# Kernel tuning notes

Hardware: AMD Instinct MI355X
Metric: run time of the kernel (lower is better)

Reference implementation:

```python
import jax, jax.numpy as jnp
import numpy as np

B, L, NV = 16, 512, 64
D = 512
PATCH_LEN, STRIDE, PADDING = 16, 8, 8
N_PATCH = (L - PATCH_LEN) // STRIDE + 2  # 64
PRED = 192
MEM = 8192
TOPK = 8
NHEAD = 4
NORM_CONST = 0.4
HEAD_NF = D * N_PATCH


def _pos_emb(n, d):
    pos = np.arange(n)[:, None].astype(np.float32)
    div = np.exp(np.arange(0, d, 2).astype(np.float32) * (-np.log(10000.0) / d))
    pe = np.zeros((n, d), np.float32)
    pe[:, 0::2] = np.sin(pos * div)
    pe[:, 1::2] = np.cos(pos * div)
    return jnp.asarray(pe)

POS = _pos_emb(N_PATCH, D)


def gelu(x):
    return jax.nn.gelu(x, approximate=False)  # torch nn.GELU default = exact erf


def setup_inputs() -> dict:
    key = jax.random.key(0)
    ks = jax.random.split(key, 16)
    s = lambda i, shape, scale=0.02: jax.random.normal(ks[i], shape, jnp.float32) * scale
    return dict(
        x_enc=jax.random.normal(ks[0], (B, L, NV), jnp.float32),
        W_val=s(1, (PATCH_LEN, D), 0.05),
        mem_bank=s(2, (MEM, D), 1.0),
        W_m1=s(3, (D, 2 * D)), b_m1=jnp.zeros((2 * D,), jnp.float32),
        W_m2=s(4, (2 * D, D)), b_m2=jnp.zeros((D,), jnp.float32),
        W_q=s(5, (D, D)), b_q=jnp.zeros((D,), jnp.float32),
        W_k=s(6, (D, D)), b_k=jnp.zeros((D,), jnp.float32),
        W_v=s(7, (D, D)), b_v=jnp.zeros((D,), jnp.float32),
        W_o=s(8, (D, D)), b_o=jnp.zeros((D,), jnp.float32),
        W_g1=s(9, (2 * D, D)), b_g1=jnp.zeros((D,), jnp.float32),
        W_g2=s(10, (D, 2)), b_g2=jnp.zeros((2,), jnp.float32),
        W_h=s(11, (HEAD_NF, PRED)), b_h=jnp.zeros((PRED,), jnp.float32),
        W_f1=s(12, (PRED, 2 * PRED)), b_f1=jnp.zeros((2 * PRED,), jnp.float32),
        W_f2=s(13, (2 * PRED, PRED)), b_f2=jnp.zeros((PRED,), jnp.float32),
    )


def reference(x_enc, W_val, mem_bank, W_m1, b_m1, W_m2, b_m2,
              W_q, b_q, W_k, b_k, W_v, b_v, W_o, b_o,
              W_g1, b_g1, W_g2, b_g2, W_h, b_h, W_f1, b_f1, W_f2, b_f2):
    # instance normalization over the time axis (means detached in torch)
    means = jax.lax.stop_gradient(jnp.mean(x_enc, axis=1, keepdims=True))
    xc = x_enc - means
    stdev = jnp.sqrt(jnp.var(xc, axis=1, keepdims=True) + 1e-5) / NORM_CONST
    x = xc / stdev                                              # [B, L, NV]

    # patch embedding: replication pad at end, unfold, linear + sinusoidal pos
    xt = jnp.transpose(x, (0, 2, 1))                            # [B, NV, L]
    xt = jnp.concatenate([xt, jnp.repeat(xt[..., -1:], PADDING, axis=-1)], axis=-1)
    win = (jnp.arange(N_PATCH) * STRIDE)[:, None] + jnp.arange(PATCH_LEN)  # [N, P]
    patches = xt[..., win].reshape(B * NV, N_PATCH, PATCH_LEN)  # [BN, N, P]
    emb = patches @ W_val + POS                                 # [BN, N, D]

    # local memory: mean-pooled query -> matmul similarity -> top-k gather -> MLP
    qflat = jnp.mean(emb, axis=1)                               # [BN, D]
    sim = qflat @ mem_bank.T                                    # [BN, MEM]
    _, idx = jax.lax.top_k(sim, TOPK)                           # [BN, K]
    retr = mem_bank[idx]                                        # [BN, K, D]
    h = gelu(retr @ W_m1 + b_m1) @ W_m2 + b_m2
    local = jnp.mean(h, axis=1, keepdims=True) + emb            # [BN, N, D]

    # global memory: multihead self-attention (4 heads, batch_first)
    dh = D // NHEAD
    heads = lambda t: t.reshape(B * NV, N_PATCH, NHEAD, dh).transpose(0, 2, 1, 3)
    q = heads(emb @ W_q + b_q)
    k = heads(emb @ W_k + b_k)
    v = heads(emb @ W_v + b_v)
    att = jax.nn.softmax(jnp.einsum('bhqd,bhkd->bhqk', q, k) / jnp.sqrt(jnp.float32(dh)), axis=-1)
    glob = jnp.einsum('bhqk,bhkd->bhqd', att, v).transpose(0, 2, 1, 3).reshape(B * NV, N_PATCH, D)
    glob = glob @ W_o + b_o                                     # [BN, N, D]

    # gated fusion of local/global memory
    comb = jnp.concatenate([local, glob], axis=-1)              # [BN, N, 2D]
    gate = jax.nn.softmax(gelu(comb @ W_g1 + b_g1) @ W_g2 + b_g2, axis=-1)
    mem = gate[..., 0:1] * local + gate[..., 1:2] * glob        # [BN, N, D]

    # flatten -> memory head -> fusion layer with residual
    flat = mem.reshape(B * NV, HEAD_NF)
    mh = (flat @ W_h + b_h).reshape(B, NV, PRED)
    pred = gelu(gelu(mh @ W_f1 + b_f1) @ W_f2 + b_f2) + mh
    pred = jnp.transpose(pred, (0, 2, 1))                       # [B, PRED, NV]

    # denormalize
    return pred * stdev + means
```

## Files before the change

kernel.cpp:

```cpp
#include <hip/hip_runtime.h>
#include <stdint.h>

#define DEV __device__ __forceinline__

typedef uint16_t u16;
typedef __bf16 bf16x8 __attribute__((ext_vector_type(8)));
typedef float f32x4 __attribute__((ext_vector_type(4)));
typedef u16 u16x8 __attribute__((ext_vector_type(8)));

DEV float bf2f(u16 v) { return __uint_as_float(((uint32_t)v) << 16); }
DEV u16 f2bf(float f) {
  uint32_t u = __float_as_uint(f);
  u += 0x7fffu + ((u >> 16) & 1u);
  return (u16)(u >> 16);
}
DEV float gelu_f(float x) { return 0.5f * x * (1.0f + erff(x * 0.7071067811865475f)); }

DEV void gload_lds16(const u16* g, u16* l) {
  __builtin_amdgcn_global_load_lds(
      (const __attribute__((address_space(1))) void*)g,
      (__attribute__((address_space(3))) void*)l, 16, 0, 0);
}

struct __align__(16) Scratch {
  float POSb[64 * 512];
  float meanv[1024];
  float stdv[1024];
  float mh[1024 * 192];
  int idxB[8192];
  float qflat[1024 * 512];
  float gatel[65536 * 2];
  float bqkv[1536];
  u16 hmeanB[1024 * 512];
  u16 gmeanB[1024 * 1024];
  u16 WqkvT[1536 * 512];
  u16 WoT[512 * 512];
  u16 Wm1T[1024 * 512];
  u16 Wm2T[512 * 1024];
  u16 Wg1T[512 * 1024];
  u16 WhT[256 * 32768];
  u16 memdupB[8192 * 1536];
  u16 embh[65536 * 512];
  u16 qkvb[65536 * 1536];
};
__device__ Scratch g_s;

__global__ __launch_bounds__(256) void zerof_kernel(float* __restrict__ p, int n) {
  int t = blockIdx.x * 256 + threadIdx.x;
  if (t < n) p[t] = 0.f;
}
__global__ __launch_bounds__(256) void zerou8_kernel(u16* __restrict__ p, int n8) {
  int t = blockIdx.x * 256 + threadIdx.x;
  if (t < n8) *(u16x8*)(p + (long)t * 8) = (u16x8)0;
}
__global__ __launch_bounds__(256) void biasqkv_kernel(const float* __restrict__ bq,
                                                      const float* __restrict__ bk,
                                                      const float* __restrict__ bv,
                                                      float* __restrict__ o) {
  int t = blockIdx.x * 256 + threadIdx.x;
  o[t] = t < 512 ? bq[t] : (t < 1024 ? bk[t - 512] : bv[t - 1024]);
}

__global__ __launch_bounds__(256) void pos_kernel(float* __restrict__ POS) {
  int n = blockIdx.x;
  int i = threadIdx.x;
  float div = expf((float)(2 * i) * (-9.210340371976184f / 512.0f));
  float arg = (float)n * div;
  POS[n * 512 + 2 * i] = sinf(arg);
  POS[n * 512 + 2 * i + 1] = cosf(arg);
}

__global__ __launch_bounds__(256) void stats_kernel(const float* __restrict__ x_enc,
                                                    float* __restrict__ meanv,
                                                    float* __restrict__ stdv) {
  int b = blockIdx.x;
  int v = threadIdx.x & 63;
  int g = threadIdx.x >> 6;
  float s = 0.f, s2 = 0.f;
  for (int l = g; l < 512; l += 4) {
    float x = x_enc[((long)b * 512 + l) * 64 + v];
    s += x; s2 += x * x;
  }
  __shared__ float sh[2][4][64];
  sh[0][g][v] = s; sh[1][g][v] = s2;
  __syncthreads();
  if (g == 0) {
    s = sh[0][0][v] + sh[0][1][v] + sh[0][2][v] + sh[0][3][v];
    s2 = sh[1][0][v] + sh[1][1][v] + sh[1][2][v] + sh[1][3][v];
    float mu = s * (1.f / 512.f);
    float var = s2 * (1.f / 512.f) - mu * mu;
    meanv[b * 64 + v] = mu;
    stdv[b * 64 + v] = sqrtf(var + 1e-5f) * 2.5f;
  }
}

__global__ __launch_bounds__(256) void transpose_kernel(const float* __restrict__ in,
                                                        u16* __restrict__ out, int R, int C) {
  __shared__ u16 t[32][33];
  int bx = blockIdx.x * 32;
  int by = blockIdx.y * 32;
  int tx = threadIdx.x & 31, ty = threadIdx.x >> 5;
  for (int i = ty; i < 32; i += 8) t[i][tx] = f2bf(in[(long)(by + i) * C + bx + tx]);
  __syncthreads();
  for (int i = ty; i < 32; i += 8) out[(long)(bx + i) * R + by + tx] = t[tx][i];
}

__global__ __launch_bounds__(256) void emb_kernel(const float* __restrict__ x_enc,
                                                  const float* __restrict__ W_val,
                                                  const float* __restrict__ POS,
                                                  const float* __restrict__ meanv,
                                                  const float* __restrict__ stdv,
                                                  u16* __restrict__ embh,
                                                  u16* __restrict__ qsC) {
  int bn = blockIdx.x;
  int b = bn >> 6, v = bn & 63;
  int tid = threadIdx.x;
  __shared__ __align__(16) float wv[16 * 512];
  __shared__ __align__(16) float pt[64 * 16];
  for (int i = tid; i < 8192; i += 256) wv[i] = W_val[i];
  float mu = meanv[bn];
  float inv = 1.f / stdv[bn];
  for (int i = tid; i < 1024; i += 256) {
    int n = i >> 4, p = i & 15;
    int l = n * 8 + p; if (l > 511) l = 511;
    pt[i] = (x_enc[((long)b * 512 + l) * 64 + v] - mu) * inv;
  }
  __syncthreads();
  float qs0 = 0.f, qs1 = 0.f;
  int d0 = tid, d1 = tid + 256;
  for (int n = 0; n < 64; ++n) {
    float a0 = POS[n * 512 + d0], a1 = POS[n * 512 + d1];
#pragma unroll
    for (int p = 0; p < 16; ++p) {
      float pv = pt[n * 16 + p];
      a0 += pv * wv[p * 512 + d0];
      a1 += pv * wv[p * 512 + d1];
    }
    long base = ((long)bn * 64 + n) * 512;
    embh[base + d0] = f2bf(a0);
    embh[base + d1] = f2bf(a1);
    qs0 += a0; qs1 += a1;
  }
  float q0 = qs0 * (1.f / 64.f), q1 = qs1 * (1.f / 64.f);
  u16 h0 = f2bf(q0), l0 = f2bf(q0 - bf2f(h0));
  u16 h1 = f2bf(q1), l1 = f2bf(q1 - bf2f(h1));
  long qb = (long)bn * 1536;
  qsC[qb + d0] = h0; qsC[qb + 512 + d0] = l0; qsC[qb + 1024 + d0] = h0;
  qsC[qb + d1] = h1; qsC[qb + 512 + d1] = l1; qsC[qb + 1024 + d1] = h1;
}

__global__ __launch_bounds__(256) void memdup_kernel(const float* __restrict__ mb,
                                                     u16* __restrict__ md) {
  int t = blockIdx.x * 256 + threadIdx.x;
  int n = t >> 6, k8 = (t & 63) * 8;
  const float* src = mb + (long)n * 512 + k8;
  u16x8 hi, lo;
#pragma unroll
  for (int z = 0; z < 8; ++z) {
    float m = src[z];
    u16 h = f2bf(m);
    hi[z] = h;
    lo[z] = f2bf(m - bf2f(h));
  }
  long base = (long)n * 1536 + k8;
  *(u16x8*)(md + base) = hi;
  *(u16x8*)(md + base + 512) = hi;
  *(u16x8*)(md + base + 1024) = lo;
}

template <int EPI>
__global__ __launch_bounds__(256) void gemm_nt(const u16* __restrict__ Ag,
                                               const u16* __restrict__ Bt,
                                               const float* __restrict__ bias,
                                               void* __restrict__ C,
                                               int lda, int ldb, int K, int Nreal, int ldc,
                                               int nT, long zstride) {
  __shared__ __align__(16) u16 smem[2 * 128 * 64];
  u16* As = smem;
  u16* Bs = smem + 8192;
  const int tid = threadIdx.x;
  const int id = blockIdx.x;
  const int xcd = id & 7;
  const int kk = id >> 3;
  const long bm = (long)((kk / nT) * 8 + xcd) * 128;
  const long bnn = (long)(kk % nT) * 128;
  const long koff = (long)blockIdx.z * K;
  const int lane = tid & 63;
  const int w = tid >> 6;
  const int wm = (w & 1) * 64;
  const int wn = (w >> 1) * 64;
  const int r16 = lane & 15;
  const int q4 = lane >> 4;

  f32x4 acc[4][4] = {};

  const u16* ap[4];
  const u16* bp[4];
  u16* al[4];
  u16* bl[4];
#pragma unroll
  for (int j = 0; j < 4; ++j) {
    int cid = (j * 4 + w) * 64 + lane;
    int r = cid >> 3;
    int g = (cid & 7) ^ (r & 7);
    ap[j] = Ag + (bm + r) * lda + koff + g * 8;
    bp[j] = Bt + (bnn + r) * ldb + koff + g * 8;
    al[j] = As + cid * 8;
    bl[j] = Bs + cid * 8;
  }

  for (int k0 = 0; k0 < K; k0 += 64) {
#pragma unroll
    for (int j = 0; j < 4; ++j) gload_lds16(ap[j] + k0, al[j]);
#pragma unroll
    for (int j = 0; j < 4; ++j) gload_lds16(bp[j] + k0, bl[j]);
    __syncthreads();
#pragma unroll
    for (int sub = 0; sub < 2; ++sub) {
      const int gg = q4 + sub * 4;
      bf16x8 av[4], bv[4];
#pragma unroll
      for (int i = 0; i < 4; ++i) {
        int r = wm + i * 16 + r16;
        av[i] = *reinterpret_cast<const bf16x8*>(As + (r * 8 + (gg ^ (r & 7))) * 8);
      }
#pragma unroll
      for (int j2 = 0; j2 < 4; ++j2) {
        int r = wn + j2 * 16 + r16;
        bv[j2] = *reinterpret_cast<const bf16x8*>(Bs + (r * 8 + (gg ^ (r & 7))) * 8);
      }
#pragma unroll
      for (int i = 0; i < 4; ++i)
#pragma unroll
        for (int j2 = 0; j2 < 4; ++j2)
          acc[i][j2] = __builtin_amdgcn_mfma_f32_16x16x32_bf16(av[i], bv[j2], acc[i][j2], 0, 0, 0);
    }
    __syncthreads();
  }

  if (EPI == 3) {
    float* Cz = (float*)C + (long)blockIdx.z * zstride;
    float* epf = (float*)smem + w * 2048;
#pragma unroll
    for (int half = 0; half < 2; ++half) {
#pragma unroll
      for (int i = 0; i < 2; ++i)
#pragma unroll
        for (int j = 0; j < 4; ++j)
#pragma unroll
          for (int r = 0; r < 4; ++r)
            epf[(i * 16 + q4 * 4 + r) * 64 + j * 16 + r16] = acc[half * 2 + i][j][r];
      __syncthreads();
#pragma unroll
      for (int v2 = 0; v2 < 8; ++v2) {
        int idx = v2 * 64 + lane;
        int row = idx >> 4, c4 = (idx & 15) * 4;
        f32x4 vec = *(const f32x4*)(epf + row * 64 + c4);
        long grow = bm + wm + half * 32 + row;
        int gcol = (int)bnn + wn + c4;
        if (gcol < Nreal) *(f32x4*)(Cz + grow * (long)ldc + gcol) = vec;
      }
      __syncthreads();
    }
  } else {
    u16* ep = smem + w * 2304;
    float bcol[4];
#pragma unroll
    for (int j = 0; j < 4; ++j) bcol[j] = bias[bnn + wn + j * 16 + r16];
#pragma unroll
    for (int half = 0; half < 2; ++half) {
#pragma unroll
      for (int i = 0; i < 2; ++i)
#pragma unroll
        for (int j = 0; j < 4; ++j)
#pragma unroll
          for (int r = 0; r < 4; ++r) {
            float v = acc[half * 2 + i][j][r] + bcol[j];
            if (EPI == 1) v = gelu_f(v);
            ep[(i * 16 + q4 * 4 + r) * 72 + j * 16 + r16] = f2bf(v);
          }
      __syncthreads();
#pragma unroll
      for (int v2 = 0; v2 < 4; ++v2) {
        int row = v2 * 8 + (lane >> 3);
        int c8 = (lane & 7) * 8;
        u16x8 vec = *(const u16x8*)(ep + row * 72 + c8);
        long grow = bm + wm + half * 32 + row;
        int gcol = (int)bnn + wn + c8;
        if (gcol < Nreal) *(u16x8*)((u16*)C + grow * (long)ldc + gcol) = vec;
      }
      __syncthreads();
    }
  }
}

DEV bool better(float v1, int i1, float v2, int i2) {
  return v1 > v2 || (v1 == v2 && i1 < i2);
}
__global__ __launch_bounds__(256) void topk_kernel(const float* __restrict__ sim,
                                                   int* __restrict__ idxout) {
  const int bn = blockIdx.x;
  const int tid = threadIdx.x;
  const float* row = sim + (long)bn * 8192;
  float bv[8]; int bi[8];
#pragma unroll
  for (int r = 0; r < 8; ++r) { bv[r] = -3.0e38f; bi[r] = 0x7fffffff; }
  for (int n = tid; n < 8192; n += 256) {
    float v = row[n];
    if (better(v, n, bv[7], bi[7])) {
      bv[7] = v; bi[7] = n;
      for (int r = 7; r > 0; --r) {
        if (!better(bv[r], bi[r], bv[r - 1], bi[r - 1])) break;
        float tv = bv[r]; bv[r] = bv[r - 1]; bv[r - 1] = tv;
        int ti = bi[r]; bi[r] = bi[r - 1]; bi[r - 1] = ti;
      }
    }
  }
  __shared__ float lv[256 * 8];
  __shared__ int li[256 * 8];
#pragma unroll
  for (int r = 0; r < 8; ++r) { lv[tid * 8 + r] = bv[r]; li[tid * 8 + r] = bi[r]; }
  __syncthreads();
  for (int step = 128; step >= 1; step >>= 1) {
    if (tid < step) {
      float av[8], xv[8]; int ai[8], xi[8];
#pragma unroll
      for (int r = 0; r < 8; ++r) {
        av[r] = lv[tid * 8 + r]; ai[r] = li[tid * 8 + r];
        xv[r] = lv[(tid + step) * 8 + r]; xi[r] = li[(tid + step) * 8 + r];
      }
      int ia = 0, ib = 0;
      float mv[8]; int mi[8];
#pragma unroll
      for (int r = 0; r < 8; ++r) {
        if (better(av[ia], ai[ia], xv[ib], xi[ib])) { mv[r] = av[ia]; mi[r] = ai[ia]; ++ia; }
        else { mv[r] = xv[ib]; mi[r] = xi[ib]; ++ib; }
      }
#pragma unroll
      for (int r = 0; r < 8; ++r) { lv[tid * 8 + r] = mv[r]; li[tid * 8 + r] = mi[r]; }
    }
    __syncthreads();
  }
  if (tid < 8) idxout[bn * 8 + tid] = li[tid];
}

__global__ __launch_bounds__(256) void gather_kernel(const float* __restrict__ mb,
                                                     const int* __restrict__ idx,
                                                     u16* __restrict__ retrB) {
  int t = blockIdx.x * 256 + threadIdx.x;
  int m = t >> 6;
  int c8 = (t & 63) * 8;
  long r = idx[m];
  if (r < 0) r = 0;
  if (r > 8191) r = 8191;
  const float* src = mb + r * 512 + c8;
  u16x8 o;
#pragma unroll
  for (int z = 0; z < 8; ++z) o[z] = f2bf(src[z]);
  *(u16x8*)(retrB + (long)m * 512 + c8) = o;
}

__global__ __launch_bounds__(256) void gmean_kernel(const u16* __restrict__ hid,
                                                    u16* __restrict__ gmeanB) {
  int t = blockIdx.x * 256 + threadIdx.x;
  int bn = t >> 7, j8 = (t & 127) * 8;
  float s[8] = {};
#pragma unroll
  for (int k = 0; k < 8; ++k) {
    u16x8 v = *(const u16x8*)(hid + (long)(bn * 8 + k) * 1024 + j8);
#pragma unroll
    for (int z = 0; z < 8; ++z) s[z] += bf2f(v[z]);
  }
  u16x8 o;
#pragma unroll
  for (int z = 0; z < 8; ++z) o[z] = f2bf(s[z] * 0.125f);
  *(u16x8*)(gmeanB + (long)bn * 1024 + j8) = o;
}

__global__ __launch_bounds__(256) void attn_kernel(u16* __restrict__ qkvb) {
  __shared__ __align__(16) u16 smem[26752];
  u16* Qs = smem;
  u16* Ks = smem + 8704;
  float* ss = (float*)(smem + 8704);
  u16* ps = smem;
  u16* Os = smem;
  u16* Vb = smem + 17408;
  float* red = (float*)(smem + 25728);
  const int bn = blockIdx.x, h = blockIdx.y;
  const int tid = threadIdx.x;
  const int lane = tid & 63, w = tid >> 6;
  const int r16 = lane & 15, q4 = lane >> 4;
  const long base = (long)bn * 64 * 1536 + h * 128;

  for (int c = tid; c < 1024; c += 256) {
    int r = c >> 4, c8 = (c & 15) * 8;
    u16x8 vq = *(const u16x8*)(qkvb + base + (long)r * 1536 + c8);
    u16x8 vk = *(const u16x8*)(qkvb + base + (long)r * 1536 + 512 + c8);
    u16x8 vv = *(const u16x8*)(qkvb + base + (long)r * 1536 + 1024 + c8);
    *(u16x8*)(Qs + r * 136 + c8) = vq;
    *(u16x8*)(Ks + r * 136 + c8) = vk;
    int kt = r >> 5, q4t = (r >> 3) & 3, e = r & 7;
    int nt = c8 >> 4, rb = c8 & 15;
    int vbase = (nt * 2 + kt) * 520 + (q4t * 16 + rb) * 8 + e;
#pragma unroll
    for (int z = 0; z < 8; ++z) Vb[vbase + z * 8] = vv[z];
  }
  __syncthreads();

  const int m0 = w * 16;
  f32x4 accS[4] = {};
#pragma unroll
  for (int k0 = 0; k0 < 128; k0 += 32) {
    bf16x8 av = *(const bf16x8*)(Qs + (m0 + r16) * 136 + k0 + q4 * 8);
#pragma unroll
    for (int j = 0; j < 4; ++j) {
      bf16x8 bvf = *(const bf16x8*)(Ks + (j * 16 + r16) * 136 + k0 + q4 * 8);
      accS[j] = __builtin_amdgcn_mfma_f32_16x16x32_bf16(av, bvf, accS[j], 0, 0, 0);
    }
  }
  __syncthreads();
  const float scale = 0.08838834764831845f;
#pragma unroll
  for (int j = 0; j < 4; ++j)
#pragma unroll
    for (int r = 0; r < 4; ++r)
      ss[(m0 + q4 * 4 + r) * 66 + j * 16 + r16] = accS[j][r] * scale;
  __syncthreads();

  {
    int r = tid >> 2, p = tid & 3;
    float* row = ss + r * 66 + p * 16;
    float mx = -3.0e38f;
#pragma unroll
    for (int c2 = 0; c2 < 16; ++c2) mx = fmaxf(mx, row[c2]);
    red[r * 4 + p] = mx;
    __syncthreads();
    float m4 = fmaxf(fmaxf(red[r * 4], red[r * 4 + 1]),
                     fmaxf(red[r * 4 + 2], red[r * 4 + 3]));
    float s = 0.f;
#pragma unroll
    for (int c2 = 0; c2 < 16; ++c2) {
      float e = expf(row[c2] - m4);
      row[c2] = e;
      s += e;
    }
    red[256 + r * 4 + p] = s;
    __syncthreads();
    float inv = 1.f / (red[256 + r * 4] + red[256 + r * 4 + 1] +
                       red[256 + r * 4 + 2] + red[256 + r * 4 + 3]);
    u16x8 o0, o1;
#pragma unroll
    for (int z = 0; z < 8; ++z) {
      o0[z] = f2bf(row[z] * inv);
      o1[z] = f2bf(row[8 + z] * inv);
    }
    *(u16x8*)(ps + r * 72 + p * 16) = o0;
    *(u16x8*)(ps + r * 72 + p * 16 + 8) = o1;
  }
  __syncthreads();

  bf16x8 av0 = *(const bf16x8*)(ps + (m0 + r16) * 72 + q4 * 8);
  bf16x8 av1 = *(const bf16x8*)(ps + (m0 + r16) * 72 + 32 + q4 * 8);
  __syncthreads();
#pragma unroll
  for (int nt = 0; nt < 8; ++nt) {
    f32x4 accO = {};
    bf16x8 bv0 = *(const bf16x8*)(Vb + (nt * 2 + 0) * 520 + lane * 8);
    bf16x8 bv1 = *(const bf16x8*)(Vb + (nt * 2 + 1) * 520 + lane * 8);
    accO = __builtin_amdgcn_mfma_f32_16x16x32_bf16(av0, bv0, accO, 0, 0, 0);
    accO = __builtin_amdgcn_mfma_f32_16x16x32_bf16(av1, bv1, accO, 0, 0, 0);
#pragma unroll
    for (int r = 0; r < 4; ++r) {
      int i = m0 + q4 * 4 + r;
      int col = nt * 16 + r16;
      Os[i * 128 + (col ^ (q4 << 4))] = f2bf(accO[r]);
    }
  }
  __syncthreads();
#pragma unroll
  for (int z = 0; z < 4; ++z) {
    int idx = z * 256 + tid;
    int row = idx >> 4, c8 = (idx & 15) * 8;
    int c8s = c8 ^ (((row >> 2) & 3) << 4);
    u16x8 vec = *(const u16x8*)(Os + row * 128 + c8s);
    *(u16x8*)(qkvb + base + (long)row * 1536 + c8) = vec;
  }
}

__global__ __launch_bounds__(256) void local_kernel(u16* __restrict__ embh,
                                                    const u16* __restrict__ hmeanB) {
  long t = (long)blockIdx.x * 256 + threadIdx.x;
  long e8 = t * 8;
  long m = e8 >> 9;
  int d = (int)(e8 & 511);
  int bn = (int)(m >> 6);
  u16x8 a = *(const u16x8*)(embh + e8);
  u16x8 b = *(const u16x8*)(hmeanB + (long)bn * 512 + d);
  u16x8 o;
#pragma unroll
  for (int z = 0; z < 8; ++z) o[z] = f2bf(bf2f(a[z]) + bf2f(b[z]));
  *(u16x8*)(embh + e8) = o;
}

__global__ __launch_bounds__(256) void gemm_cat(const u16* __restrict__ A1,
                                                const u16* __restrict__ A2,
                                                const u16* __restrict__ Bt,
                                                const float* __restrict__ bias,
                                                const float* __restrict__ W_g2,
                                                float* __restrict__ gatel,
                                                int lda1, int lda2, int nT) {
  __shared__ __align__(16) u16 smem[2 * 128 * 64];
  u16* As = smem;
  u16* Bs = smem + 8192;
  const int tid = threadIdx.x;
  const int id = blockIdx.x;
  const int xcd = id & 7;
  const int kk = id >> 3;
  const long bm = (long)((kk / nT) * 8 + xcd) * 128;
  const long bnn = (long)(kk % nT) * 128;
  const int lane = tid & 63;
  const int w = tid >> 6;
  const int wm = (w & 1) * 64;
  const int wn = (w >> 1) * 64;
  const int r16 = lane & 15;
  const int q4 = lane >> 4;

  f32x4 acc[4][4] = {};

  const u16* ap1[4];
  const u16* ap2[4];
  const u16* bp[4];
  u16* al[4];
  u16* bl[4];
#pragma unroll
  for (int j = 0; j < 4; ++j) {
    int cid = (j * 4 + w) * 64 + lane;
    int r = cid >> 3;
    int g = (cid & 7) ^ (r & 7);
    ap1[j] = A1 + (bm + r) * lda1 + g * 8;
    ap2[j] = A2 + (bm + r) * lda2 + g * 8;
    bp[j] = Bt + (bnn + r) * 1024 + g * 8;
    al[j] = As + cid * 8;
    bl[j] = Bs + cid * 8;
  }

  for (int k0 = 0; k0 < 1024; k0 += 64) {
    if (k0 < 512) {
#pragma unroll
      for (int j = 0; j < 4; ++j) gload_lds16(ap1[j] + k0, al[j]);
    } else {
#pragma unroll
      for (int j = 0; j < 4; ++j) gload_lds16(ap2[j] + (k0 - 512), al[j]);
    }
#pragma unroll
    for (int j = 0; j < 4; ++j) gload_lds16(bp[j] + k0, bl[j]);
    __syncthreads();
#pragma unroll
    for (int sub = 0; sub < 2; ++sub) {
      const int gg = q4 + sub * 4;
      bf16x8 av[4], bv[4];
#pragma unroll
      for (int i = 0; i < 4; ++i) {
        int r = wm + i * 16 + r16;
        av[i] = *reinterpret_cast<const bf16x8*>(As + (r * 8 + (gg ^ (r & 7))) * 8);
      }
#pragma unroll
      for (int j2 = 0; j2 < 4; ++j2) {
        int r = wn + j2 * 16 + r16;
        bv[j2] = *reinterpret_cast<const bf16x8*>(Bs + (r * 8 + (gg ^ (r & 7))) * 8);
      }
#pragma unroll
      for (int i = 0; i < 4; ++i)
#pragma unroll
        for (int j2 = 0; j2 < 4; ++j2)
          acc[i][j2] = __builtin_amdgcn_mfma_f32_16x16x32_bf16(av[i], bv[j2], acc[i][j2], 0, 0, 0);
    }
    __syncthreads();
  }

  float bcol[4], w0[4], w1[4];
#pragma unroll
  for (int j = 0; j < 4; ++j) {
    int gc = (int)bnn + wn + j * 16 + r16;
    bcol[j] = bias[gc];
    w0[j] = W_g2[gc * 2];
    w1[j] = W_g2[gc * 2 + 1];
  }
#pragma unroll
  for (int i = 0; i < 4; ++i)
#pragma unroll
    for (int r = 0; r < 4; ++r) {
      float a0 = 0.f, a1 = 0.f;
#pragma unroll
      for (int j = 0; j < 4; ++j) {
        float h = gelu_f(acc[i][j][r] + bcol[j]);
        a0 += h * w0[j];
        a1 += h * w1[j];
      }
#pragma unroll
      for (int off = 1; off < 16; off <<= 1) {
        a0 += __shfl_xor(a0, off);
        a1 += __shfl_xor(a1, off);
      }
      if (r16 == 0) {
        long row = bm + wm + i * 16 + q4 * 4 + r;
        atomicAdd(&gatel[row * 2], a0);
        atomicAdd(&gatel[row * 2 + 1], a1);
      }
    }
}

__global__ __launch_bounds__(256) void memc_kernel(u16* __restrict__ embh,
                                                   const u16* __restrict__ qkvb,
                                                   const float* __restrict__ gatel,
                                                   const float* __restrict__ b_g2) {
  long t = (long)blockIdx.x * 256 + threadIdx.x;
  long e8 = t * 8;
  long m = e8 >> 9;
  int d = (int)(e8 & 511);
  float l0 = gatel[m * 2] + b_g2[0];
  float l1 = gatel[m * 2 + 1] + b_g2[1];
  float mx = fmaxf(l0, l1);
  float e0 = expf(l0 - mx), e1 = expf(l1 - mx);
  float inv = 1.f / (e0 + e1);
  float g0 = e0 * inv, g1 = e1 * inv;
  u16x8 loc = *(const u16x8*)(embh + e8);
  u16x8 gl = *(const u16x8*)(qkvb + m * 1536 + 512 + d);
  u16x8 o;
#pragma unroll
  for (int z = 0; z < 8; ++z) o[z] = f2bf(g0 * bf2f(loc[z]) + g1 * bf2f(gl[z]));
  *(u16x8*)(embh + e8) = o;
}

__global__ __launch_bounds__(256) void fusion_kernel(const float* __restrict__ mh16,
                                                     const float* __restrict__ b_h,
                                                     const float* __restrict__ W_f1,
                                                     const float* __restrict__ b_f1,
                                                     const float* __restrict__ W_f2,
                                                     const float* __restrict__ b_f2,
                                                     const float* __restrict__ meanv,
                                                     const float* __restrict__ stdv,
                                                     float* __restrict__ out) {
  int bn = blockIdx.x;
  int tid = threadIdx.x;
  __shared__ float mrow[192];
  __shared__ float h1[384];
  if (tid < 192) {
    float a = b_h[tid];
#pragma unroll
    for (int z = 0; z < 16; ++z) a += mh16[(long)z * 196608 + (long)bn * 192 + tid];
    mrow[tid] = a;
  }
  __syncthreads();
  for (int j = tid; j < 384; j += 256) {
    float a = b_f1[j];
    for (int i = 0; i < 192; ++i) a += mrow[i] * W_f1[i * 384 + j];
    h1[j] = gelu_f(a);
  }
  __syncthreads();
  if (tid < 192) {
    float a = b_f2[tid];
    for (int j = 0; j < 384; ++j) a += h1[j] * W_f2[j * 192 + tid];
    float o = gelu_f(a) + mrow[tid];
    int b = bn >> 6, v = bn & 63;
    out[((long)b * 192 + tid) * 64 + v] = o * stdv[bn] + meanv[bn];
  }
}

extern "C" void kernel_launch(void* const* d_in, const int* in_sizes, int n_in,
                              void* d_out, int out_size, void* d_ws, size_t ws_size,
                              hipStream_t stream) {
  (void)in_sizes; (void)n_in; (void)out_size; (void)d_ws; (void)ws_size;
  const float* x_enc = (const float*)d_in[0];
  const float* W_val = (const float*)d_in[1];
  const float* mem_bank = (const float*)d_in[2];
  const float* W_m1 = (const float*)d_in[3];
  const float* b_m1 = (const float*)d_in[4];
  const float* W_m2 = (const float*)d_in[5];
  const float* b_m2 = (const float*)d_in[6];
  const float* W_q = (const float*)d_in[7];
  const float* b_q = (const float*)d_in[8];
  const float* W_k = (const float*)d_in[9];
  const float* b_k = (const float*)d_in[10];
  const float* W_v = (const float*)d_in[11];
  const float* b_v = (const float*)d_in[12];
  const float* W_o = (const float*)d_in[13];
  const float* b_o = (const float*)d_in[14];
  const float* W_g1 = (const float*)d_in[15];
  const float* b_g1 = (const float*)d_in[16];
  const float* W_g2 = (const float*)d_in[17];
  const float* b_g2 = (const float*)d_in[18];
  const float* W_h = (const float*)d_in[19];
  const float* b_h = (const float*)d_in[20];
  const float* W_f1 = (const float*)d_in[21];
  const float* b_f1 = (const float*)d_in[22];
  const float* W_f2 = (const float*)d_in[23];
  const float* b_f2 = (const float*)d_in[24];

  void* sp = nullptr;
  hipGetSymbolAddress(&sp, HIP_SYMBOL(g_s));
  Scratch* S = (Scratch*)sp;
  float* simB = (float*)S->qkvb;
  u16* qsC = S->qkvb + (size_t)16 * 1024 * 1024;
  u16* retrB = S->qkvb + (size_t)18 * 1024 * 1024;
  u16* hiddenB = S->qkvb + (size_t)24 * 1024 * 1024;
  float* mh16 = (float*)S->qkvb;

  pos_kernel<<<64, 256, 0, stream>>>(S->POSb);
  stats_kernel<<<16, 256, 0, stream>>>(x_enc, S->meanv, S->stdv);
  zerof_kernel<<<512, 256, 0, stream>>>(S->gatel, 65536 * 2);
  zerou8_kernel<<<1024, 256, 0, stream>>>(S->WhT + (size_t)192 * 32768, 64 * 32768 / 8);
  biasqkv_kernel<<<6, 256, 0, stream>>>(b_q, b_k, b_v, S->bqkv);
  transpose_kernel<<<dim3(16, 16), 256, 0, stream>>>(W_q, S->WqkvT, 512, 512);
  transpose_kernel<<<dim3(16, 16), 256, 0, stream>>>(W_k, S->WqkvT + 512 * 512, 512, 512);
  transpose_kernel<<<dim3(16, 16), 256, 0, stream>>>(W_v, S->WqkvT + 2 * 512 * 512, 512, 512);
  transpose_kernel<<<dim3(16, 16), 256, 0, stream>>>(W_o, S->WoT, 512, 512);
  transpose_kernel<<<dim3(32, 16), 256, 0, stream>>>(W_m1, S->Wm1T, 512, 1024);
  transpose_kernel<<<dim3(16, 32), 256, 0, stream>>>(W_m2, S->Wm2T, 1024, 512);
  transpose_kernel<<<dim3(16, 32), 256, 0, stream>>>(W_g1, S->Wg1T, 1024, 512);
  transpose_kernel<<<dim3(6, 1024), 256, 0, stream>>>(W_h, S->WhT, 32768, 192);
  memdup_kernel<<<2048, 256, 0, stream>>>(mem_bank, S->memdupB);

  emb_kernel<<<1024, 256, 0, stream>>>(x_enc, W_val, S->POSb, S->meanv, S->stdv,
                                       S->embh, qsC);
  gemm_nt<3><<<512, 256, 0, stream>>>(qsC, S->memdupB, nullptr, simB,
                                      1536, 1536, 1536, 8192, 8192, 64, 0L);
  topk_kernel<<<1024, 256, 0, stream>>>(simB, S->idxB);
  gather_kernel<<<2048, 256, 0, stream>>>(mem_bank, S->idxB, retrB);
  gemm_nt<1><<<512, 256, 0, stream>>>(retrB, S->Wm1T, b_m1, hiddenB,
                                      512, 512, 512, 1024, 1024, 8, 0L);
  gmean_kernel<<<512, 256, 0, stream>>>(hiddenB, S->gmeanB);
  gemm_nt<0><<<32, 256, 0, stream>>>(S->gmeanB, S->Wm2T, b_m2, S->hmeanB,
                                     1024, 1024, 1024, 512, 512, 4, 0L);
  gemm_nt<0><<<6144, 256, 0, stream>>>(S->embh, S->WqkvT, S->bqkv, S->qkvb,
                                       512, 512, 512, 1536, 1536, 12, 0L);
  local_kernel<<<16384, 256, 0, stream>>>(S->embh, S->hmeanB);
  attn_kernel<<<dim3(1024, 4), 256, 0, stream>>>(S->qkvb);
  gemm_nt<0><<<2048, 256, 0, stream>>>(S->qkvb, S->WoT, b_o, S->qkvb + 512,
                                       1536, 512, 512, 512, 1536, 4, 0L);
  gemm_cat<<<2048, 256, 0, stream>>>(S->embh, S->qkvb + 512, S->Wg1T, b_g1,
                                     W_g2, S->gatel, 512, 1536, 4);
  memc_kernel<<<16384, 256, 0, stream>>>(S->embh, S->qkvb, S->gatel, b_g2);
  gemm_nt<3><<<dim3(16, 1, 16), 256, 0, stream>>>(S->embh, S->WhT, nullptr, mh16,
                                                  32768, 32768, 2048, 192, 192, 2,
                                                  196608L);
  fusion_kernel<<<1024, 256, 0, stream>>>(mh16, b_h, W_f1, b_f1, W_f2, b_f2,
                                          S->meanv, S->stdv, (float*)d_out);
}
```

Baseline: 1.093 ms.

## Double-buffer LDS in sim and gate GEMMs; pack local/global into contiguous buffer

Adds a gemm_db kernel that double-buffers the A/B tiles in LDS, issuing the next k-step's global-to-LDS loads before computing the current one, and waits with explicit vmcnt counts. It is used for the similarity GEMM and the gate GEMM. To remove the two-source k-loop in the old concatenated gate GEMM, local and global memory are now written into one interleaved [M,1024] buffer, and attention output goes to a separate obuf. This costs extra scratch memory and doubles the LDS use per block, which may lower occupancy.

```diff
diff --git a/kernel.cpp b/kernel.cpp
--- a/kernel.cpp
+++ b/kernel.cpp
@@ -41,6 +41,8 @@
   u16 WhT[256 * 32768];
   u16 memdupB[8192 * 1536];
   u16 embh[65536 * 512];
+  u16 locglob[65536 * 1024];
+  u16 obuf[65536 * 512];
   u16 qkvb[65536 * 1536];
 };
 __device__ Scratch g_s;
@@ -294,6 +296,152 @@
   }
 }
 
+template <int EPI>
+__global__ __launch_bounds__(256) void gemm_db(const u16* __restrict__ Ag,
+                                               const u16* __restrict__ Bt,
+                                               const float* __restrict__ bias,
+                                               void* __restrict__ C,
+                                               const float* __restrict__ W_g2,
+                                               float* __restrict__ gatel,
+                                               int lda, int ldb, int K, int Nreal, int ldc,
+                                               int nT) {
+  __shared__ __align__(16) u16 smem[4 * 128 * 64];
+  const int tid = threadIdx.x;
+  const int id = blockIdx.x;
+  const int xcd = id & 7;
+  const int kk = id >> 3;
+  const long bm = (long)((kk / nT) * 8 + xcd) * 128;
+  const long bnn = (long)(kk % nT) * 128;
+  const int lane = tid & 63;
+  const int w = tid >> 6;
+  const int wm = (w & 1) * 64;
+  const int wn = (w >> 1) * 64;
+  const int r16 = lane & 15;
+  const int q4 = lane >> 4;
+
+  f32x4 acc[4][4] = {};
+
+  const u16* ap[4];
+  const u16* bp[4];
+  int ao[4], bo[4];
+#pragma unroll
+  for (int j = 0; j < 4; ++j) {
+    int cid = (j * 4 + w) * 64 + lane;
+    int r = cid >> 3;
+    int g = (cid & 7) ^ (r & 7);
+    ap[j] = Ag + (bm + r) * lda + g * 8;
+    bp[j] = Bt + (bnn + r) * ldb + g * 8;
+    ao[j] = cid * 8;
+    bo[j] = 8192 + cid * 8;
+  }
+
+#pragma unroll
+  for (int j = 0; j < 4; ++j) gload_lds16(ap[j], smem + ao[j]);
+#pragma unroll
+  for (int j = 0; j < 4; ++j) gload_lds16(bp[j], smem + bo[j]);
+
+  const int nsteps = K >> 6;
+  for (int s = 0; s < nsteps; ++s) {
+    const int cur = s & 1;
+    u16* buf = smem + cur * 16384;
+    if (s + 1 < nsteps) {
+      u16* nb = smem + (cur ^ 1) * 16384;
+      const int k1 = (s + 1) << 6;
+#pragma unroll
+      for (int j = 0; j < 4; ++j) gload_lds16(ap[j] + k1, nb + ao[j]);
+#pragma unroll
+      for (int j = 0; j < 4; ++j) gload_lds16(bp[j] + k1, nb + bo[j]);
+      asm volatile("s_waitcnt vmcnt(8)" ::: "memory");
+    } else {
+      asm volatile("s_waitcnt vmcnt(0)" ::: "memory");
+    }
+    __builtin_amdgcn_sched_barrier(0);
+    __builtin_amdgcn_s_barrier();
+    __builtin_amdgcn_sched_barrier(0);
+    u16* As = buf;
+    u16* Bs = buf + 8192;
+#pragma unroll
+    for (int sub = 0; sub < 2; ++sub) {
+      const int gg = q4 + sub * 4;
+      bf16x8 av[4], bv[4];
+#pragma unroll
+      for (int i = 0; i < 4; ++i) {
+        int r = wm + i * 16 + r16;
+        av[i] = *reinterpret_cast<const bf16x8*>(As + (r * 8 + (gg ^ (r & 7))) * 8);
+      }
+#pragma unroll
+      for (int j2 = 0; j2 < 4; ++j2) {
+        int r = wn + j2 * 16 + r16;
+        bv[j2] = *reinterpret_cast<const bf16x8*>(Bs + (r * 8 + (gg ^ (r & 7))) * 8);
+      }
+#pragma unroll
+      for (int i = 0; i < 4; ++i)
+#pragma unroll
+        for (int j2 = 0; j2 < 4; ++j2)
+          acc[i][j2] = __builtin_amdgcn_mfma_f32_16x16x32_bf16(av[i], bv[j2], acc[i][j2], 0, 0, 0);
+    }
+    __builtin_amdgcn_sched_barrier(0);
+    __builtin_amdgcn_s_barrier();
+    __builtin_amdgcn_sched_barrier(0);
+  }
+
+  if (EPI == 3) {
+    float* epf = (float*)smem + w * 2048;
+#pragma unroll
+    for (int half = 0; half < 2; ++half) {
+#pragma unroll
+      for (int i = 0; i < 2; ++i)
+#pragma unroll
+        for (int j = 0; j < 4; ++j)
+#pragma unroll
+          for (int r = 0; r < 4; ++r)
+            epf[(i * 16 + q4 * 4 + r) * 64 + j * 16 + r16] = acc[half * 2 + i][j][r];
+      __syncthreads();
+#pragma unroll
+      for (int v2 = 0; v2 < 8; ++v2) {
+        int idx = v2 * 64 + lane;
+        int row = idx >> 4, c4 = (idx & 15) * 4;
+        f32x4 vec = *(const f32x4*)(epf + row * 64 + c4);
+        long grow = bm + wm + half * 32 + row;
+        int gcol = (int)bnn + wn + c4;
+        if (gcol < Nreal) *(f32x4*)((float*)C + grow * (long)ldc + gcol) = vec;
+      }
+      __syncthreads();
+    }
+  } else {
+    float bcol[4], w0[4], w1[4];
+#pragma unroll
+    for (int j = 0; j < 4; ++j) {
+      int gc = (int)bnn + wn + j * 16 + r16;
+      bcol[j] = bias[gc];
+      w0[j] = W_g2[gc * 2];
+      w1[j] = W_g2[gc * 2 + 1];
+    }
+#pragma unroll
+    for (int i = 0; i < 4; ++i)
+#pragma unroll
+      for (int r = 0; r < 4; ++r) {
+        float a0 = 0.f, a1 = 0.f;
+#pragma unroll
+        for (int j = 0; j < 4; ++j) {
+          float h = gelu_f(acc[i][j][r] + bcol[j]);
+          a0 += h * w0[j];
+          a1 += h * w1[j];
+        }
+#pragma unroll
+        for (int off = 1; off < 16; off <<= 1) {
+          a0 += __shfl_xor(a0, off);
+          a1 += __shfl_xor(a1, off);
+        }
+        if (r16 == 0) {
+          long row = bm + wm + i * 16 + q4 * 4 + r;
+          atomicAdd(&gatel[row * 2], a0);
+          atomicAdd(&gatel[row * 2 + 1], a1);
+        }
+      }
+  }
+}
+
 DEV bool better(float v1, int i1, float v2, int i2) {
   return v1 > v2 || (v1 == v2 && i1 < i2);
 }
@@ -377,7 +525,8 @@
   *(u16x8*)(gmeanB + (long)bn * 1024 + j8) = o;
 }
 
-__global__ __launch_bounds__(256) void attn_kernel(u16* __restrict__ qkvb) {
+__global__ __launch_bounds__(256) void attn_kernel(const u16* __restrict__ qkvb,
+                                                   u16* __restrict__ obuf) {
   __shared__ __align__(16) u16 smem[26752];
   u16* Qs = smem;
   u16* Ks = smem + 8704;
@@ -483,12 +632,13 @@
     int row = idx >> 4, c8 = (idx & 15) * 8;
     int c8s = c8 ^ (((row >> 2) & 3) << 4);
     u16x8 vec = *(const u16x8*)(Os + row * 128 + c8s);
-    *(u16x8*)(qkvb + base + (long)row * 1536 + c8) = vec;
-  }
-}
-
-__global__ __launch_bounds__(256) void local_kernel(u16* __restrict__ embh,
-                                                    const u16* __restrict__ hmeanB) {
+    *(u16x8*)(obuf + ((long)bn * 64 + row) * 512 + h * 128 + c8) = vec;
+  }
+}
+
+__global__ __launch_bounds__(256) void local_kernel(const u16* __restrict__ embh,
+                                                    const u16* __restrict__ hmeanB,
+                                                    u16* __restrict__ locglob) {
   long t = (long)blockIdx.x * 256 + threadIdx.x;
   long e8 = t * 8;
   long m = e8 >> 9;
@@ -499,119 +649,11 @@
   u16x8 o;
 #pragma unroll
   for (int z = 0; z < 8; ++z) o[z] = f2bf(bf2f(a[z]) + bf2f(b[z]));
-  *(u16x8*)(embh + e8) = o;
-}
-
-__global__ __launch_bounds__(256) void gemm_cat(const u16* __restrict__ A1,
-                                                const u16* __restrict__ A2,
-                                                const u16* __restrict__ Bt,
-                                                const float* __restrict__ bias,
-                                                const float* __restrict__ W_g2,
-                                                float* __restrict__ gatel,
-                                                int lda1, int lda2, int nT) {
-  __shared__ __align__(16) u16 smem[2 * 128 * 64];
-  u16* As = smem;
-  u16* Bs = smem + 8192;
-  const int tid = threadIdx.x;
-  const int id = blockIdx.x;
-  const int xcd = id & 7;
-  const int kk = id >> 3;
-  const long bm = (long)((kk / nT) * 8 + xcd) * 128;
-  const long bnn = (long)(kk % nT) * 128;
-  const int lane = tid & 63;
-  const int w = tid >> 6;
-  const int wm = (w & 1) * 64;
-  const int wn = (w >> 1) * 64;
-  const int r16 = lane & 15;
-  const int q4 = lane >> 4;
-
-  f32x4 acc[4][4] = {};
-
-  const u16* ap1[4];
-  const u16* ap2[4];
-  const u16* bp[4];
-  u16* al[4];
-  u16* bl[4];
-#pragma unroll
-  for (int j = 0; j < 4; ++j) {
-    int cid = (j * 4 + w) * 64 + lane;
-    int r = cid >> 3;
-    int g = (cid & 7) ^ (r & 7);
-    ap1[j] = A1 + (bm + r) * lda1 + g * 8;
-    ap2[j] = A2 + (bm + r) * lda2 + g * 8;
-    bp[j] = Bt + (bnn + r) * 1024 + g * 8;
-    al[j] = As + cid * 8;
-    bl[j] = Bs + cid * 8;
-  }
-
-  for (int k0 = 0; k0 < 1024; k0 += 64) {
-    if (k0 < 512) {
-#pragma unroll
-      for (int j = 0; j < 4; ++j) gload_lds16(ap1[j] + k0, al[j]);
-    } else {
-#pragma unroll
-      for (int j = 0; j < 4; ++j) gload_lds16(ap2[j] + (k0 - 512), al[j]);
-    }
-#pragma unroll
-    for (int j = 0; j < 4; ++j) gload_lds16(bp[j] + k0, bl[j]);
-    __syncthreads();
-#pragma unroll
-    for (int sub = 0; sub < 2; ++sub) {
-      const int gg = q4 + sub * 4;
-      bf16x8 av[4], bv[4];
-#pragma unroll
-      for (int i = 0; i < 4; ++i) {
-        int r = wm + i * 16 + r16;
-        av[i] = *reinterpret_cast<const bf16x8*>(As + (r * 8 + (gg ^ (r & 7))) * 8);
-      }
-#pragma unroll
-      for (int j2 = 0; j2 < 4; ++j2) {
-        int r = wn + j2 * 16 + r16;
-        bv[j2] = *reinterpret_cast<const bf16x8*>(Bs + (r * 8 + (gg ^ (r & 7))) * 8);
-      }
-#pragma unroll
-      for (int i = 0; i < 4; ++i)
-#pragma unroll
-        for (int j2 = 0; j2 < 4; ++j2)
-          acc[i][j2] = __builtin_amdgcn_mfma_f32_16x16x32_bf16(av[i], bv[j2], acc[i][j2], 0, 0, 0);
-    }
-    __syncthreads();
-  }
-
-  float bcol[4], w0[4], w1[4];
-#pragma unroll
-  for (int j = 0; j < 4; ++j) {
-    int gc = (int)bnn + wn + j * 16 + r16;
-    bcol[j] = bias[gc];
-    w0[j] = W_g2[gc * 2];
-    w1[j] = W_g2[gc * 2 + 1];
-  }
-#pragma unroll
-  for (int i = 0; i < 4; ++i)
-#pragma unroll
-    for (int r = 0; r < 4; ++r) {
-      float a0 = 0.f, a1 = 0.f;
-#pragma unroll
-      for (int j = 0; j < 4; ++j) {
-        float h = gelu_f(acc[i][j][r] + bcol[j]);
-        a0 += h * w0[j];
-        a1 += h * w1[j];
-      }
-#pragma unroll
-      for (int off = 1; off < 16; off <<= 1) {
-        a0 += __shfl_xor(a0, off);
-        a1 += __shfl_xor(a1, off);
-      }
-      if (r16 == 0) {
-        long row = bm + wm + i * 16 + q4 * 4 + r;
-        atomicAdd(&gatel[row * 2], a0);
-        atomicAdd(&gatel[row * 2 + 1], a1);
-      }
-    }
+  *(u16x8*)(locglob + m * 1024 + d) = o;
 }
 
 __global__ __launch_bounds__(256) void memc_kernel(u16* __restrict__ embh,
-                                                   const u16* __restrict__ qkvb,
+                                                   const u16* __restrict__ locglob,
                                                    const float* __restrict__ gatel,
                                                    const float* __restrict__ b_g2) {
   long t = (long)blockIdx.x * 256 + threadIdx.x;
@@ -624,8 +666,8 @@
   float e0 = expf(l0 - mx), e1 = expf(l1 - mx);
   float inv = 1.f / (e0 + e1);
   float g0 = e0 * inv, g1 = e1 * inv;
-  u16x8 loc = *(const u16x8*)(embh + e8);
-  u16x8 gl = *(const u16x8*)(qkvb + m * 1536 + 512 + d);
+  u16x8 loc = *(const u16x8*)(locglob + m * 1024 + d);
+  u16x8 gl = *(const u16x8*)(locglob + m * 1024 + 512 + d);
   u16x8 o;
 #pragma unroll
   for (int z = 0; z < 8; ++z) o[z] = f2bf(g0 * bf2f(loc[z]) + g1 * bf2f(gl[z]));
@@ -723,8 +765,8 @@
 
   emb_kernel<<<1024, 256, 0, stream>>>(x_enc, W_val, S->POSb, S->meanv, S->stdv,
                                        S->embh, qsC);
-  gemm_nt<3><<<512, 256, 0, stream>>>(qsC, S->memdupB, nullptr, simB,
-                                      1536, 1536, 1536, 8192, 8192, 64, 0L);
+  gemm_db<3><<<512, 256, 0, stream>>>(qsC, S->memdupB, nullptr, simB, nullptr, nullptr,
+                                      1536, 1536, 1536, 8192, 8192, 64);
   topk_kernel<<<1024, 256, 0, stream>>>(simB, S->idxB);
   gather_kernel<<<2048, 256, 0, stream>>>(mem_bank, S->idxB, retrB);
   gemm_nt<1><<<512, 256, 0, stream>>>(retrB, S->Wm1T, b_m1, hiddenB,
@@ -734,13 +776,13 @@
                                      1024, 1024, 1024, 512, 512, 4, 0L);
   gemm_nt<0><<<6144, 256, 0, stream>>>(S->embh, S->WqkvT, S->bqkv, S->qkvb,
                                        512, 512, 512, 1536, 1536, 12, 0L);
-  local_kernel<<<16384, 256, 0, stream>>>(S->embh, S->hmeanB);
-  attn_kernel<<<dim3(1024, 4), 256, 0, stream>>>(S->qkvb);
-  gemm_nt<0><<<2048, 256, 0, stream>>>(S->qkvb, S->WoT, b_o, S->qkvb + 512,
-                                       1536, 512, 512, 512, 1536, 4, 0L);
-  gemm_cat<<<2048, 256, 0, stream>>>(S->embh, S->qkvb + 512, S->Wg1T, b_g1,
-                                     W_g2, S->gatel, 512, 1536, 4);
-  memc_kernel<<<16384, 256, 0, stream>>>(S->embh, S->qkvb, S->gatel, b_g2);
+  local_kernel<<<16384, 256, 0, stream>>>(S->embh, S->hmeanB, S->locglob);
+  attn_kernel<<<dim3(1024, 4), 256, 0, stream>>>(S->qkvb, S->obuf);
+  gemm_nt<0><<<2048, 256, 0, stream>>>(S->obuf, S->WoT, b_o, S->locglob + 512,
+                                       512, 512, 512, 512, 1024, 4, 0L);
+  gemm_db<4><<<2048, 256, 0, stream>>>(S->locglob, S->Wg1T, b_g1, nullptr,
+                                       W_g2, S->gatel, 1024, 1024, 1024, 512, 0, 4);
+  memc_kernel<<<16384, 256, 0, stream>>>(S->embh, S->locglob, S->gatel, b_g2);
   gemm_nt<3><<<dim3(16, 1, 16), 256, 0, stream>>>(S->embh, S->WhT, nullptr, mh16,
                                                   32768, 32768, 2048, 192, 192, 2,
                                                   196608L);
```

New measurement: 958.8 us. 1.14x faster.
